# Optimization experiments

Measured on AMD Instinct MI355X. Metric: run time of the kernel, lower is better.

## Reference

```python
import jax, jax.numpy as jnp
import numpy as np

WEIGHT = 1.0  # config['weight']


def setup_inputs() -> dict:
    key = jax.random.key(0)
    ks = jax.random.split(key, 10)
    B, N, S, C, D, E, H, V = 8, 4096, 512, 16, 1024, 256, 1024, 100000
    return {
        "span_vecs": jax.random.normal(ks[0], (B, N, D), jnp.float32),
        "ent_table": jax.random.normal(ks[1], (V, E), jnp.float32) * 0.02,
        "W1": jax.random.normal(ks[2], (D + E, H), jnp.float32) * (1.0 / np.sqrt(D + E)),
        "b1": jnp.zeros((H,), jnp.float32),
        "W2": jax.random.normal(ks[3], (H,), jnp.float32) * (1.0 / np.sqrt(H)),
        "b2": jnp.zeros((), jnp.float32),
        "targets_all": jax.random.uniform(ks[4], (B, N, C), jnp.float32),
        "linker_indices": jax.random.randint(ks[5], (B, S), 0, N, jnp.int32),
        "candidates_all": jax.random.randint(ks[6], (B, N, C), 0, V, jnp.int32),
        "candidate_lengths_all": jax.random.randint(ks[7], (B, N), 0, C + 1, jnp.int32),
    }


def reference(span_vecs, ent_table, W1, b1, W2, b2, targets_all,
              linker_indices, candidates_all, candidate_lengths_all):
    D = span_vecs.shape[-1]
    C = candidates_all.shape[-1]
    idx = linker_indices  # [B, S]

    # batched_index_select gathers over the span axis
    candidates = jnp.take_along_axis(candidates_all, idx[:, :, None], axis=1)        # [B,S,C] int
    lengths = jnp.take_along_axis(candidate_lengths_all, idx, axis=1)                # [B,S] int
    targets = jnp.take_along_axis(targets_all, idx[:, :, None], axis=1)              # [B,S,C]
    linker_vecs = jnp.take_along_axis(span_vecs, idx[:, :, None], axis=1)            # [B,S,D]

    cand_vecs = ent_table[candidates]                                                # [B,S,C,E]

    # layers: Linear(D+E,H) -> ReLU -> (dropout=identity in eval) -> Linear(H,1)
    # fused: split W1 so the [B,S,C,D+E] expanded concat is never materialized
    W1s, W1e = W1[:D], W1[D:]
    h_span = jnp.einsum('bsd,dh->bsh', linker_vecs, W1s)                             # [B,S,H]
    h_cand = jnp.einsum('bsce,eh->bsch', cand_vecs, W1e)                             # [B,S,C,H]
    h = jax.nn.relu(h_span[:, :, None, :] + h_cand + b1)
    scores = jnp.einsum('bsch,h->bsc', h, W2) + b2                                   # [B,S,C]

    # create_candidate_mask
    mask = (jnp.arange(C)[None, None, :] < lengths[:, :, None]).astype(scores.dtype)

    # BCEWithLogitsLoss(reduction='none'), masked sum * weight
    bce = jnp.maximum(scores, 0.0) - scores * targets + jnp.log1p(jnp.exp(-jnp.abs(scores)))
    loss = (mask * bce).sum() * WEIGHT

    predictions = jnp.argmax(scores - (1.0 - mask) * 1e23, axis=-1)                  # [B,S]
    return loss, scores, predictions
```

## Files before the change

### kernel.cpp

```cpp
#include <hip/hip_runtime.h>
#include <math.h>


typedef short short8 __attribute__((ext_vector_type(8)));
typedef _Float16 half8v __attribute__((ext_vector_type(8)));
typedef float f32x16 __attribute__((ext_vector_type(16)));

static __device__ inline unsigned short f2bf(float x) {
  unsigned u = __float_as_uint(x);
  unsigned r = (u + 0x7FFFu + ((u >> 16) & 1u)) >> 16;
  return (unsigned short)r;
}
static __device__ inline float bf2f(unsigned short b) {
  return __uint_as_float(((unsigned)b) << 16);
}
static __device__ inline unsigned short f2h(float x) {
  _Float16 h = (_Float16)x;
  return *(unsigned short*)&h;
}

#define GLD_TO_LDS(gp, lp)                                          \
  __builtin_amdgcn_global_load_lds(                                 \
      (const __attribute__((address_space(1))) void*)(gp),          \
      (__attribute__((address_space(3))) void*)(lp), 16, 0, 0)

__global__ __launch_bounds__(256) void k_prep2(const int* __restrict__ linker,
                                               const int* __restrict__ cand_all,
                                               int* __restrict__ cand_ids,
                                               int* __restrict__ span_rows) {
  int g = blockIdx.x * 256 + threadIdx.x;
  int pair = g >> 4;
  int b = pair >> 9;
  int i = linker[pair];
  cand_ids[g] = cand_all[(((size_t)b << 12) + (size_t)i) * 16 + (g & 15)];
  if (g < 4096) span_rows[g] = ((g >> 9) << 12) + linker[g];
}

template <int LOG4>
__global__ __launch_bounds__(256) void k_gsplit(const float* __restrict__ src,
                                                const int* __restrict__ rows,
                                                unsigned short* __restrict__ hi,
                                                unsigned short* __restrict__ lo) {
  int f = blockIdx.x * 256 + threadIdx.x;
  int row = f >> LOG4;
  int c4 = f & ((1 << LOG4) - 1);
  const float4 v =
      *((const float4*)(src + ((size_t)rows[row] << (LOG4 + 2))) + c4);
  unsigned short h0 = f2bf(v.x), h1 = f2bf(v.y), h2 = f2bf(v.z), h3 = f2bf(v.w);
  unsigned short l0 = f2bf(v.x - bf2f(h0)), l1 = f2bf(v.y - bf2f(h1));
  unsigned short l2 = f2bf(v.z - bf2f(h2)), l3 = f2bf(v.w - bf2f(h3));
  *(ushort4*)(hi + ((size_t)f << 2)) = make_ushort4(h0, h1, h2, h3);
  *(ushort4*)(lo + ((size_t)f << 2)) = make_ushort4(l0, l1, l2, l3);
}

template <int LOG4>
__global__ __launch_bounds__(256) void k_gh(const float* __restrict__ src,
                                            const int* __restrict__ rows,
                                            unsigned short* __restrict__ dst) {
  int f = blockIdx.x * 256 + threadIdx.x;
  int row = f >> LOG4;
  int c4 = f & ((1 << LOG4) - 1);
  const float4 v =
      *((const float4*)(src + ((size_t)rows[row] << (LOG4 + 2))) + c4);
  *(ushort4*)(dst + ((size_t)f << 2)) =
      make_ushort4(f2h(v.x), f2h(v.y), f2h(v.z), f2h(v.w));
}

__global__ __launch_bounds__(256) void k_w1t(const float* __restrict__ W1,
                                             unsigned short* __restrict__ sThi,
                                             unsigned short* __restrict__ sTlo,
                                             unsigned short* __restrict__ eT16) {
  __shared__ float t[32][33];
  int n0 = blockIdx.x * 32, k0 = blockIdx.y * 32;
  int rr = threadIdx.x >> 5, cc = threadIdx.x & 31;
#pragma unroll
  for (int i = 0; i < 4; ++i)
    t[rr + 8 * i][cc] = W1[(size_t)(k0 + rr + 8 * i) * 1024 + n0 + cc];
  __syncthreads();
#pragma unroll
  for (int i = 0; i < 4; ++i) {
    int nl = rr + 8 * i;
    float v = t[cc][nl];
    int n = n0 + nl, k = k0 + cc;
    if (k0 < 1024) {
      unsigned short h = f2bf(v);
      unsigned short l = f2bf(v - bf2f(h));
      sThi[(size_t)n * 1024 + k] = h;
      sTlo[(size_t)n * 1024 + k] = l;
    } else {
      eT16[(size_t)n * 256 + (k - 1024)] = f2h(v);
    }
  }
}

template <int KSTEPS, int RLA, int RLB>
__global__ __launch_bounds__(256, 2) void k_g32(
    const unsigned short* __restrict__ Ahi, const unsigned short* __restrict__ Alo,
    const unsigned short* __restrict__ Bhi, const unsigned short* __restrict__ Blo,
    float* __restrict__ Out) {
  const int tid = threadIdx.x;
  const int l = tid & 63;
  const int w = tid >> 6;
  const int wm = w >> 1, wn = w & 1;
  const int id = blockIdx.x;
  const int m8 = id & 7;
  const int cb = (id >> 3) & 7;
  const int q = id >> 6;
  const int row0 = ((q << 3) + m8) << 7;
  const int col0 = cb << 7;

  __shared__ unsigned short lds[32768];

  f32x16 acc[2][2];
#pragma unroll
  for (int i = 0; i < 2; ++i)
#pragma unroll
    for (int j = 0; j < 2; ++j)
#pragma unroll
      for (int k = 0; k < 16; ++k) acc[i][j][k] = 0.f;

  const int ar0 = tid >> 2, ap0 = tid & 3;
  const int al0c = ap0 ^ ((ar0 >> 1) & 3);
  const int ar1 = (tid + 256) >> 2;
  const int al1c = ap0 ^ ((ar1 >> 1) & 3);
  const size_t aoff0 = (size_t)(row0 + ar0) * RLA + al0c * 8;
  const size_t aoff1 = (size_t)(row0 + ar1) * RLA + al1c * 8;
  const size_t boff0 = (size_t)(col0 + ar0) * RLB + al0c * 8;
  const size_t boff1 = (size_t)(col0 + ar1) * RLB + al1c * 8;
  const int w512 = w * 512;

  {
    unsigned short* b = lds;
    GLD_TO_LDS(Ahi + aoff0, b + w512);
    GLD_TO_LDS(Ahi + aoff1, b + 2048 + w512);
    GLD_TO_LDS(Alo + aoff0, b + 4096 + w512);
    GLD_TO_LDS(Alo + aoff1, b + 6144 + w512);
    GLD_TO_LDS(Bhi + boff0, b + 8192 + w512);
    GLD_TO_LDS(Bhi + boff1, b + 10240 + w512);
    GLD_TO_LDS(Blo + boff0, b + 12288 + w512);
    GLD_TO_LDS(Blo + boff1, b + 14336 + w512);
  }
  asm volatile("s_waitcnt vmcnt(0)" ::: "memory");
  __builtin_amdgcn_s_barrier();
  asm volatile("" ::: "memory");

  for (int ks = 0; ks < KSTEPS; ++ks) {
    if (ks + 1 < KSTEPS) {
      const int k0 = (ks + 1) * 32;
      unsigned short* b = lds + (((ks + 1) & 1) << 14);
      GLD_TO_LDS(Ahi + aoff0 + k0, b + w512);
      GLD_TO_LDS(Ahi + aoff1 + k0, b + 2048 + w512);
      GLD_TO_LDS(Alo + aoff0 + k0, b + 4096 + w512);
      GLD_TO_LDS(Alo + aoff1 + k0, b + 6144 + w512);
      GLD_TO_LDS(Bhi + boff0 + k0, b + 8192 + w512);
      GLD_TO_LDS(Bhi + boff1 + k0, b + 10240 + w512);
      GLD_TO_LDS(Blo + boff0 + k0, b + 12288 + w512);
      GLD_TO_LDS(Blo + boff1 + k0, b + 14336 + w512);
    }

    const unsigned short* cbuf = lds + ((ks & 1) << 14);
#pragma unroll
    for (int kc = 0; kc < 2; ++kc) {
      const int kg = kc * 2 + (l >> 5);
      short8 ah[2], alv[2], bh[2], bl[2];
#pragma unroll
      for (int it = 0; it < 2; ++it) {
        int r = wm * 64 + it * 32 + (l & 31);
        int off = r * 32 + ((kg ^ ((r >> 1) & 3)) << 3);
        ah[it] = *(const short8*)(cbuf + off);
        alv[it] = *(const short8*)(cbuf + 4096 + off);
      }
#pragma unroll
      for (int jt = 0; jt < 2; ++jt) {
        int r = wn * 64 + jt * 32 + (l & 31);
        int off = r * 32 + ((kg ^ ((r >> 1) & 3)) << 3);
        bh[jt] = *(const short8*)(cbuf + 8192 + off);
        bl[jt] = *(const short8*)(cbuf + 12288 + off);
      }
#pragma unroll
      for (int it = 0; it < 2; ++it)
#pragma unroll
        for (int jt = 0; jt < 2; ++jt) {
          acc[it][jt] = __builtin_amdgcn_mfma_f32_32x32x16_bf16(
              ah[it], bh[jt], acc[it][jt], 0, 0, 0);
          acc[it][jt] = __builtin_amdgcn_mfma_f32_32x32x16_bf16(
              ah[it], bl[jt], acc[it][jt], 0, 0, 0);
          acc[it][jt] = __builtin_amdgcn_mfma_f32_32x32x16_bf16(
              alv[it], bh[jt], acc[it][jt], 0, 0, 0);
        }
    }

    if (ks + 1 < KSTEPS) {
      asm volatile("s_waitcnt vmcnt(0)" ::: "memory");
      __builtin_amdgcn_s_barrier();
      asm volatile("" ::: "memory");
    }
  }

#pragma unroll
  for (int it = 0; it < 2; ++it) {
    int mb = row0 + wm * 64 + it * 32 + 4 * (l >> 5);
#pragma unroll
    for (int jt = 0; jt < 2; ++jt) {
      int n = col0 + wn * 64 + jt * 32 + (l & 31);
#pragma unroll
      for (int rg = 0; rg < 16; ++rg) {
        int m = mb + (rg & 3) + 8 * (rg >> 2);
        Out[(size_t)m * 1024 + n] = acc[it][jt][rg];
      }
    }
  }
}

__global__ __launch_bounds__(256, 4) void k_gf16(
    const unsigned short* __restrict__ A,
    const unsigned short* __restrict__ Bt,
    const float* __restrict__ HsIn, const float* __restrict__ b1,
    const float* __restrict__ W2, float* __restrict__ Out) {
  const int tid = threadIdx.x;
  const int l = tid & 63;
  const int w = tid >> 6;
  const int wm = w >> 1, wn = w & 1;
  const int id = blockIdx.x;
  const int m8 = id & 7;
  const int cb = (id >> 3) & 7;
  const int q = id >> 6;
  const int row0 = ((q << 3) + m8) << 7;
  const int col0 = cb << 7;

  __shared__ unsigned short lds[16384];

  f32x16 acc[2][2];
#pragma unroll
  for (int i = 0; i < 2; ++i)
#pragma unroll
    for (int j = 0; j < 2; ++j)
#pragma unroll
      for (int k = 0; k < 16; ++k) acc[i][j][k] = 0.f;

  const int ar0 = tid >> 2, ap0 = tid & 3;
  const int al0c = ap0 ^ ((ar0 >> 1) & 3);
  const int ar1 = (tid + 256) >> 2;
  const int al1c = ap0 ^ ((ar1 >> 1) & 3);
  const size_t aoff0 = (size_t)(row0 + ar0) * 256 + al0c * 8;
  const size_t aoff1 = (size_t)(row0 + ar1) * 256 + al1c * 8;
  const size_t boff0 = (size_t)(col0 + ar0) * 256 + al0c * 8;
  const size_t boff1 = (size_t)(col0 + ar1) * 256 + al1c * 8;
  const int w512 = w * 512;

  GLD_TO_LDS(A + aoff0, lds + w512);
  GLD_TO_LDS(A + aoff1, lds + 2048 + w512);
  GLD_TO_LDS(Bt + boff0, lds + 4096 + w512);
  GLD_TO_LDS(Bt + boff1, lds + 6144 + w512);
  asm volatile("s_waitcnt vmcnt(0)" ::: "memory");
  __builtin_amdgcn_s_barrier();
  asm volatile("" ::: "memory");

#pragma unroll 2
  for (int ks = 0; ks < 8; ++ks) {
    if (ks + 1 < 8) {
      const int k0 = (ks + 1) * 32;
      unsigned short* b = lds + (((ks + 1) & 1) << 13);
      GLD_TO_LDS(A + aoff0 + k0, b + w512);
      GLD_TO_LDS(A + aoff1 + k0, b + 2048 + w512);
      GLD_TO_LDS(Bt + boff0 + k0, b + 4096 + w512);
      GLD_TO_LDS(Bt + boff1 + k0, b + 6144 + w512);
    }

    const unsigned short* cbuf = lds + ((ks & 1) << 13);
#pragma unroll
    for (int kc = 0; kc < 2; ++kc) {
      const int kg = kc * 2 + (l >> 5);
      half8v av[2], bv[2];
#pragma unroll
      for (int it = 0; it < 2; ++it) {
        int r = wm * 64 + it * 32 + (l & 31);
        int off = r * 32 + ((kg ^ ((r >> 1) & 3)) << 3);
        av[it] = *(const half8v*)(cbuf + off);
      }
#pragma unroll
      for (int jt = 0; jt < 2; ++jt) {
        int r = wn * 64 + jt * 32 + (l & 31);
        int off = r * 32 + ((kg ^ ((r >> 1) & 3)) << 3);
        bv[jt] = *(const half8v*)(cbuf + 4096 + off);
      }
#pragma unroll
      for (int it = 0; it < 2; ++it)
#pragma unroll
        for (int jt = 0; jt < 2; ++jt)
          acc[it][jt] = __builtin_amdgcn_mfma_f32_32x32x16_f16(
              av[it], bv[jt], acc[it][jt], 0, 0, 0);
    }

    if (ks + 1 < 8) {
      asm volatile("s_waitcnt vmcnt(0)" ::: "memory");
      __builtin_amdgcn_s_barrier();
      asm volatile("" ::: "memory");
    }
  }

  float sv[2][16];
#pragma unroll
  for (int it = 0; it < 2; ++it) {
#pragma unroll
    for (int rg = 0; rg < 16; ++rg) sv[it][rg] = 0.f;
    const int p0 = (row0 + wm * 64 + it * 32) >> 4;
#pragma unroll
    for (int jt = 0; jt < 2; ++jt) {
      int n = col0 + wn * 64 + jt * 32 + (l & 31);
      float b1v = b1[n], w2v = W2[n];
      float add0 = HsIn[(size_t)p0 * 1024 + n] + b1v;
      float add1 = HsIn[(size_t)(p0 + 1) * 1024 + n] + b1v;
#pragma unroll
      for (int rg = 0; rg < 16; ++rg) {
        float h = fmaxf(acc[it][jt][rg] + (rg < 8 ? add0 : add1), 0.f);
        sv[it][rg] = fmaf(h, w2v, sv[it][rg]);
      }
    }
  }
  __syncthreads();
  float* scf = (float*)lds;
  const int cc0 = l & 31, lh4 = 4 * (l >> 5);
#pragma unroll
  for (int it = 0; it < 2; ++it)
#pragma unroll
    for (int rg = 0; rg < 16; ++rg) {
      int row = (rg & 3) + 8 * (rg >> 2) + lh4;
      scf[((w * 2 + it) * 32 + row) * 32 + ((cc0 + row) & 31)] = sv[it][rg];
    }
  __syncthreads();
  int gr = tid >> 1, h = tid & 1;
  int r = gr & 31, itv = (gr >> 5) & 1, wmv = gr >> 6;
  const float* sa = scf + ((wmv * 4 + itv) * 32 + r) * 32;
  const float* sb = scf + ((wmv * 4 + 2 + itv) * 32 + r) * 32;
  float sum = 0.f;
#pragma unroll
  for (int j = 0; j < 16; ++j) {
    int cidx = (h * 16 + j + r) & 31;
    sum += sa[cidx] + sb[cidx];
  }
  sum += __shfl_xor(sum, 1, 64);
  if (h == 0) Out[(size_t)cb * 65536 + row0 + gr] = sum;
}

__global__ __launch_bounds__(64) void k_final8(const float* __restrict__ score8,
                                               const float* __restrict__ b2p,
                                               const float* __restrict__ targets_all,
                                               const int* __restrict__ linker,
                                               const int* __restrict__ len_all,
                                               float* __restrict__ out) {
  int p = blockIdx.x * 64 + threadIdx.x;
  float b2 = b2p[0];
  int b = p >> 9;
  int i = linker[p];
  int len = len_all[(b << 12) + i];
  const float* tg = targets_all + ((((size_t)b << 12) + (size_t)i) << 4);

  float loss = 0.f;
  float best = -INFINITY;
  int bc = 0;
#pragma unroll
  for (int c = 0; c < 16; ++c) {
    float sc = b2;
#pragma unroll
    for (int c8 = 0; c8 < 8; ++c8) sc += score8[c8 * 65536 + p * 16 + c];
    out[1 + p * 16 + c] = sc;
    float val;
    if (c < len) {
      float t = tg[c];
      loss += fmaxf(sc, 0.f) - sc * t + log1pf(expf(-fabsf(sc)));
      val = sc;
    } else {
      val = sc - 1e23f;
    }
    if (val > best) { best = val; bc = c; }
  }
  out[1 + 65536 + p] = (float)bc;

  for (int off = 32; off > 0; off >>= 1) loss += __shfl_down(loss, off, 64);
  if (threadIdx.x == 0) atomicAdd(out, loss);
}

#define BM 128
#define BN 128
#define BK 16
#define PAD 4

__global__ __launch_bounds__(256) void k_prep(const int* __restrict__ linker,
                                              const int* __restrict__ cand_all,
                                              int* __restrict__ cand_ids) {
  int g = blockIdx.x * 256 + threadIdx.x;
  int pair = g >> 4;
  int c = g & 15;
  int b = pair >> 9;
  int i = linker[pair];
  cand_ids[g] = cand_all[(((size_t)b << 12) + (size_t)i) * 16 + c];
}

__global__ __launch_bounds__(256) void k_hs(const float* __restrict__ span,
                                            const float* __restrict__ W1,
                                            const int* __restrict__ linker,
                                            float* __restrict__ Hs) {
  const int tid = threadIdx.x;
  const int tx = tid & 15, ty = tid >> 4;
  const int row0 = blockIdx.y * BM;
  const int col0 = blockIdx.x * BN;
  __shared__ float As[BK][BM + PAD];
  __shared__ float Bs[BK][BN + PAD];
  __shared__ int rows_g[BM];
  if (tid < BM) {
    int m = row0 + tid;
    int b = m >> 9;
    rows_g[tid] = (b << 12) + linker[m];
  }
  __syncthreads();
  float acc[8][8] = {};
  for (int k0 = 0; k0 < 1024; k0 += BK) {
#pragma unroll
    for (int ll = 0; ll < 2; ++ll) {
      int f = tid + ll * 256;
      int r = f >> 2;
      int kk = (f & 3) << 2;
      const float4 v = *(const float4*)(span + (size_t)rows_g[r] * 1024 + k0 + kk);
      As[kk + 0][r] = v.x; As[kk + 1][r] = v.y;
      As[kk + 2][r] = v.z; As[kk + 3][r] = v.w;
    }
#pragma unroll
    for (int ll = 0; ll < 2; ++ll) {
      int f = tid + ll * 256;
      int kk = f >> 5;
      int nn = (f & 31) << 2;
      *(float4*)&Bs[kk][nn] = *(const float4*)(W1 + (size_t)(k0 + kk) * 1024 + col0 + nn);
    }
    __syncthreads();
#pragma unroll
    for (int k = 0; k < BK; ++k) {
      float a[8], b[8];
      *(float4*)&a[0] = *(const float4*)&As[k][ty * 8];
      *(float4*)&a[4] = *(const float4*)&As[k][ty * 8 + 4];
      *(float4*)&b[0] = *(const float4*)&Bs[k][tx * 8];
      *(float4*)&b[4] = *(const float4*)&Bs[k][tx * 8 + 4];
#pragma unroll
      for (int i = 0; i < 8; ++i)
#pragma unroll
        for (int j = 0; j < 8; ++j) acc[i][j] = fmaf(a[i], b[j], acc[i][j]);
    }
    __syncthreads();
  }
#pragma unroll
  for (int i = 0; i < 8; ++i) {
    int m = row0 + ty * 8 + i;
    float* dst = Hs + (size_t)m * 1024 + col0 + tx * 8;
    *(float4*)dst = *(float4*)&acc[i][0];
    *(float4*)(dst + 4) = *(float4*)&acc[i][4];
  }
}

__global__ __launch_bounds__(256) void k_hc(const float* __restrict__ ent,
                                            const float* __restrict__ W1,
                                            const int* __restrict__ cand_ids,
                                            const float* __restrict__ Hs,
                                            const float* __restrict__ b1,
                                            const float* __restrict__ W2,
                                            float* __restrict__ score_ws) {
  const int tid = threadIdx.x;
  const int tx = tid & 15, ty = tid >> 4;
  const int row0 = blockIdx.y * BM;
  const int col0 = blockIdx.x * BN;
  __shared__ float As[BK][BM + PAD];
  __shared__ float Bs[BK][BN + PAD];
  __shared__ int rows_g[BM];
  __shared__ float red[BM][17];
  if (tid < BM) rows_g[tid] = cand_ids[row0 + tid];
  __syncthreads();
  float acc[8][8] = {};
  for (int k0 = 0; k0 < 256; k0 += BK) {
#pragma unroll
    for (int ll = 0; ll < 2; ++ll) {
      int f = tid + ll * 256;
      int r = f >> 2;
      int kk = (f & 3) << 2;
      const float4 v = *(const float4*)(ent + (size_t)rows_g[r] * 256 + k0 + kk);
      As[kk + 0][r] = v.x; As[kk + 1][r] = v.y;
      As[kk + 2][r] = v.z; As[kk + 3][r] = v.w;
    }
#pragma unroll
    for (int ll = 0; ll < 2; ++ll) {
      int f = tid + ll * 256;
      int kk = f >> 5;
      int nn = (f & 31) << 2;
      *(float4*)&Bs[kk][nn] =
          *(const float4*)(W1 + (size_t)(1024 + k0 + kk) * 1024 + col0 + nn);
    }
    __syncthreads();
#pragma unroll
    for (int k = 0; k < BK; ++k) {
      float a[8], b[8];
      *(float4*)&a[0] = *(const float4*)&As[k][ty * 8];
      *(float4*)&a[4] = *(const float4*)&As[k][ty * 8 + 4];
      *(float4*)&b[0] = *(const float4*)&Bs[k][tx * 8];
      *(float4*)&b[4] = *(const float4*)&Bs[k][tx * 8 + 4];
#pragma unroll
      for (int i = 0; i < 8; ++i)
#pragma unroll
        for (int j = 0; j < 8; ++j) acc[i][j] = fmaf(a[i], b[j], acc[i][j]);
    }
    __syncthreads();
  }
  const int pair = (row0 + ty * 8) >> 4;
  float hsv[8], b1v[8], w2v[8];
  {
    const float* hp = Hs + (size_t)pair * 1024 + col0 + tx * 8;
    *(float4*)&hsv[0] = *(const float4*)hp;
    *(float4*)&hsv[4] = *(const float4*)(hp + 4);
    const float* bp = b1 + col0 + tx * 8;
    *(float4*)&b1v[0] = *(const float4*)bp;
    *(float4*)&b1v[4] = *(const float4*)(bp + 4);
    const float* wp = W2 + col0 + tx * 8;
    *(float4*)&w2v[0] = *(const float4*)wp;
    *(float4*)&w2v[4] = *(const float4*)(wp + 4);
  }
#pragma unroll
  for (int i = 0; i < 8; ++i) {
    float s = 0.f;
#pragma unroll
    for (int j = 0; j < 8; ++j) {
      float h = acc[i][j] + hsv[j] + b1v[j];
      h = fmaxf(h, 0.f);
      s = fmaf(h, w2v[j], s);
    }
    red[ty * 8 + i][tx] = s;
  }
  __syncthreads();
  if (tid < BM) {
    float s = 0.f;
#pragma unroll
    for (int x = 0; x < 16; ++x) s += red[tid][x];
    atomicAdd(&score_ws[row0 + tid], s);
  }
}

__global__ __launch_bounds__(256) void k_final(const float* __restrict__ score_ws,
                                               const float* __restrict__ b2p,
                                               const float* __restrict__ targets_all,
                                               const int* __restrict__ linker,
                                               const int* __restrict__ len_all,
                                               float* __restrict__ out) {
  int p = blockIdx.x * 256 + threadIdx.x;
  float b2 = b2p[0];
  int b = p >> 9;
  int i = linker[p];
  int len = len_all[(b << 12) + i];
  const float* tg = targets_all + ((((size_t)b << 12) + (size_t)i) << 4);

  float loss = 0.f;
  float best = -INFINITY;
  int bc = 0;
#pragma unroll
  for (int c = 0; c < 16; ++c) {
    float sc = score_ws[p * 16 + c] + b2;
    out[1 + p * 16 + c] = sc;
    float val;
    if (c < len) {
      float t = tg[c];
      loss += fmaxf(sc, 0.f) - sc * t + log1pf(expf(-fabsf(sc)));
      val = sc;
    } else {
      val = sc - 1e23f;
    }
    if (val > best) { best = val; bc = c; }
  }
  out[1 + 65536 + p] = (float)bc;

  for (int off = 32; off > 0; off >>= 1) loss += __shfl_down(loss, off, 64);
  if ((threadIdx.x & 63) == 0) atomicAdd(out, loss);
}

extern "C" void kernel_launch(void* const* d_in, const int* in_sizes, int n_in,
                              void* d_out, int out_size, void* d_ws,
                              size_t ws_size, hipStream_t stream) {
  const float* span    = (const float*)d_in[0];
  const float* ent     = (const float*)d_in[1];
  const float* W1      = (const float*)d_in[2];
  const float* b1      = (const float*)d_in[3];
  const float* W2      = (const float*)d_in[4];
  const float* b2      = (const float*)d_in[5];
  const float* targets = (const float*)d_in[6];
  const int* linker    = (const int*)d_in[7];
  const int* cand_all  = (const int*)d_in[8];
  const int* len_all   = (const int*)d_in[9];
  float* out = (float*)d_out;

  char* ws = (char*)d_ws;
  float* Hs       = (float*)(ws + 0);
  float* score_ws = (float*)(ws + 16777216);
  int* cand_ids   = (int*)(ws + 17039360);
  int* span_rows  = (int*)(ws + 17301504);
  unsigned short* A1h  = (unsigned short*)(ws + 17317888);
  unsigned short* A1l  = (unsigned short*)(ws + 25706496);
  unsigned short* A2   = (unsigned short*)(ws + 34095104);
  unsigned short* sTh  = (unsigned short*)(ws + 101203968);
  unsigned short* sTl  = (unsigned short*)(ws + 103301120);
  unsigned short* eT16 = (unsigned short*)(ws + 105398272);
  const size_t NEED_MFMA = 106446848;
  float* score8 = (float*)A1h;

  hipMemsetAsync(d_out, 0, sizeof(float), stream);

  if (ws_size >= NEED_MFMA) {
    k_prep2<<<dim3(256), dim3(256), 0, stream>>>(linker, cand_all, cand_ids,
                                                 span_rows);
    k_gh<6><<<dim3(16384), dim3(256), 0, stream>>>(ent, cand_ids, A2);
    k_gsplit<8><<<dim3(4096), dim3(256), 0, stream>>>(span, span_rows, A1h, A1l);
    k_w1t<<<dim3(32, 40), dim3(256), 0, stream>>>(W1, sTh, sTl, eT16);
    k_g32<32, 1024, 1024><<<dim3(256), dim3(256), 0, stream>>>(
        A1h, A1l, sTh, sTl, Hs);
    k_gf16<<<dim3(4096), dim3(256), 0, stream>>>(A2, eT16, Hs, b1, W2, score8);
    k_final8<<<dim3(64), dim3(64), 0, stream>>>(score8, b2, targets, linker,
                                                len_all, out);
  } else {
    hipMemsetAsync(score_ws, 0, 65536 * sizeof(float), stream);
    k_prep<<<dim3(256), dim3(256), 0, stream>>>(linker, cand_all, cand_ids);
    dim3 g1(8, 32);
    k_hs<<<g1, dim3(256), 0, stream>>>(span, W1, linker, Hs);
    dim3 g2(8, 512);
    k_hc<<<g2, dim3(256), 0, stream>>>(ent, W1, cand_ids, Hs, b1, W2, score_ws);
    k_final<<<dim3(16), dim3(256), 0, stream>>>(score_ws, b2, targets, linker,
                                                len_all, out);
  }
}
```

Measured before the change: 344.7 us.

## Merge prep kernels into one launch and split-K the span GEMM across two halves

Four preprocessing kernels (index gather, entity gather to fp16, span gather with bf16 hi/lo split, W1 transpose) are folded into one block-range-dispatched kernel, so the separate index-prep pass and three launches go away. The span GEMM is split along K into two halves with 512 blocks instead of 256, which fills more CUs. The two partial Hs outputs are summed in the candidate GEMM's epilogue, which adds an extra Hs buffer read. k_final8 now reads its score partials as float4 vectors.

```diff
diff --git a/kernel.cpp b/kernel.cpp
--- a/kernel.cpp
+++ b/kernel.cpp
@@ -24,71 +24,57 @@
       (const __attribute__((address_space(1))) void*)(gp),          \
       (__attribute__((address_space(3))) void*)(lp), 16, 0, 0)
 
-__global__ __launch_bounds__(256) void k_prep2(const int* __restrict__ linker,
-                                               const int* __restrict__ cand_all,
-                                               int* __restrict__ cand_ids,
-                                               int* __restrict__ span_rows) {
-  int g = blockIdx.x * 256 + threadIdx.x;
-  int pair = g >> 4;
-  int b = pair >> 9;
-  int i = linker[pair];
-  cand_ids[g] = cand_all[(((size_t)b << 12) + (size_t)i) * 16 + (g & 15)];
-  if (g < 4096) span_rows[g] = ((g >> 9) << 12) + linker[g];
-}
-
-template <int LOG4>
-__global__ __launch_bounds__(256) void k_gsplit(const float* __restrict__ src,
-                                                const int* __restrict__ rows,
-                                                unsigned short* __restrict__ hi,
-                                                unsigned short* __restrict__ lo) {
-  int f = blockIdx.x * 256 + threadIdx.x;
-  int row = f >> LOG4;
-  int c4 = f & ((1 << LOG4) - 1);
-  const float4 v =
-      *((const float4*)(src + ((size_t)rows[row] << (LOG4 + 2))) + c4);
-  unsigned short h0 = f2bf(v.x), h1 = f2bf(v.y), h2 = f2bf(v.z), h3 = f2bf(v.w);
-  unsigned short l0 = f2bf(v.x - bf2f(h0)), l1 = f2bf(v.y - bf2f(h1));
-  unsigned short l2 = f2bf(v.z - bf2f(h2)), l3 = f2bf(v.w - bf2f(h3));
-  *(ushort4*)(hi + ((size_t)f << 2)) = make_ushort4(h0, h1, h2, h3);
-  *(ushort4*)(lo + ((size_t)f << 2)) = make_ushort4(l0, l1, l2, l3);
-}
-
-template <int LOG4>
-__global__ __launch_bounds__(256) void k_gh(const float* __restrict__ src,
-                                            const int* __restrict__ rows,
-                                            unsigned short* __restrict__ dst) {
-  int f = blockIdx.x * 256 + threadIdx.x;
-  int row = f >> LOG4;
-  int c4 = f & ((1 << LOG4) - 1);
-  const float4 v =
-      *((const float4*)(src + ((size_t)rows[row] << (LOG4 + 2))) + c4);
-  *(ushort4*)(dst + ((size_t)f << 2)) =
-      make_ushort4(f2h(v.x), f2h(v.y), f2h(v.z), f2h(v.w));
-}
-
-__global__ __launch_bounds__(256) void k_w1t(const float* __restrict__ W1,
-                                             unsigned short* __restrict__ sThi,
-                                             unsigned short* __restrict__ sTlo,
-                                             unsigned short* __restrict__ eT16) {
+__global__ __launch_bounds__(256) void k_prep_all(
+    const float* __restrict__ span, const float* __restrict__ ent,
+    const float* __restrict__ W1, const int* __restrict__ linker,
+    const int* __restrict__ cand_all, unsigned short* __restrict__ A1h,
+    unsigned short* __restrict__ A1l, unsigned short* __restrict__ A2,
+    unsigned short* __restrict__ sThi, unsigned short* __restrict__ sTlo,
+    unsigned short* __restrict__ eT16) {
   __shared__ float t[32][33];
-  int n0 = blockIdx.x * 32, k0 = blockIdx.y * 32;
-  int rr = threadIdx.x >> 5, cc = threadIdx.x & 31;
-#pragma unroll
-  for (int i = 0; i < 4; ++i)
-    t[rr + 8 * i][cc] = W1[(size_t)(k0 + rr + 8 * i) * 1024 + n0 + cc];
-  __syncthreads();
-#pragma unroll
-  for (int i = 0; i < 4; ++i) {
-    int nl = rr + 8 * i;
-    float v = t[cc][nl];
-    int n = n0 + nl, k = k0 + cc;
-    if (k0 < 1024) {
-      unsigned short h = f2bf(v);
-      unsigned short l = f2bf(v - bf2f(h));
-      sThi[(size_t)n * 1024 + k] = h;
-      sTlo[(size_t)n * 1024 + k] = l;
-    } else {
-      eT16[(size_t)n * 256 + (k - 1024)] = f2h(v);
+  const int bx = blockIdx.x;
+  if (bx < 16384) {
+    int f = bx * 256 + threadIdx.x;
+    int row = f >> 6;
+    int pair = row >> 4;
+    int b = pair >> 9;
+    int i = linker[pair];
+    int cid = cand_all[(((size_t)b << 12) + (size_t)i) * 16 + (row & 15)];
+    const float4 v = *((const float4*)(ent + ((size_t)cid << 8)) + (f & 63));
+    *(ushort4*)(A2 + ((size_t)f << 2)) =
+        make_ushort4(f2h(v.x), f2h(v.y), f2h(v.z), f2h(v.w));
+  } else if (bx < 20480) {
+    int f = (bx - 16384) * 256 + threadIdx.x;
+    int row = f >> 8;
+    int b = row >> 9;
+    int srow = (b << 12) + linker[row];
+    const float4 v = *((const float4*)(span + ((size_t)srow << 10)) + (f & 255));
+    unsigned short h0 = f2bf(v.x), h1 = f2bf(v.y), h2 = f2bf(v.z), h3 = f2bf(v.w);
+    unsigned short l0 = f2bf(v.x - bf2f(h0)), l1 = f2bf(v.y - bf2f(h1));
+    unsigned short l2 = f2bf(v.z - bf2f(h2)), l3 = f2bf(v.w - bf2f(h3));
+    *(ushort4*)(A1h + ((size_t)f << 2)) = make_ushort4(h0, h1, h2, h3);
+    *(ushort4*)(A1l + ((size_t)f << 2)) = make_ushort4(l0, l1, l2, l3);
+  } else {
+    int b2x = bx - 20480;
+    int n0 = (b2x & 31) * 32, k0 = (b2x >> 5) * 32;
+    int rr = threadIdx.x >> 5, cc = threadIdx.x & 31;
+#pragma unroll
+    for (int i = 0; i < 4; ++i)
+      t[rr + 8 * i][cc] = W1[(size_t)(k0 + rr + 8 * i) * 1024 + n0 + cc];
+    __syncthreads();
+#pragma unroll
+    for (int i = 0; i < 4; ++i) {
+      int nl = rr + 8 * i;
+      float v = t[cc][nl];
+      int n = n0 + nl, k = k0 + cc;
+      if (k0 < 1024) {
+        unsigned short h = f2bf(v);
+        unsigned short l = f2bf(v - bf2f(h));
+        sThi[(size_t)n * 1024 + k] = h;
+        sTlo[(size_t)n * 1024 + k] = l;
+      } else {
+        eT16[(size_t)n * 256 + (k - 1024)] = f2h(v);
+      }
     }
   }
 }
@@ -103,11 +89,15 @@
   const int w = tid >> 6;
   const int wm = w >> 1, wn = w & 1;
   const int id = blockIdx.x;
-  const int m8 = id & 7;
-  const int cb = (id >> 3) & 7;
-  const int q = id >> 6;
+  const int z = id >> 8;
+  const int sid = id & 255;
+  const int m8 = sid & 7;
+  const int cb = (sid >> 3) & 7;
+  const int q = sid >> 6;
   const int row0 = ((q << 3) + m8) << 7;
   const int col0 = cb << 7;
+  const int koff = z * (KSTEPS * 32);
+  Out += (size_t)z * 4194304;
 
   __shared__ unsigned short lds[32768];
 
@@ -123,10 +113,10 @@
   const int al0c = ap0 ^ ((ar0 >> 1) & 3);
   const int ar1 = (tid + 256) >> 2;
   const int al1c = ap0 ^ ((ar1 >> 1) & 3);
-  const size_t aoff0 = (size_t)(row0 + ar0) * RLA + al0c * 8;
-  const size_t aoff1 = (size_t)(row0 + ar1) * RLA + al1c * 8;
-  const size_t boff0 = (size_t)(col0 + ar0) * RLB + al0c * 8;
-  const size_t boff1 = (size_t)(col0 + ar1) * RLB + al1c * 8;
+  const size_t aoff0 = (size_t)(row0 + ar0) * RLA + al0c * 8 + koff;
+  const size_t aoff1 = (size_t)(row0 + ar1) * RLA + al1c * 8 + koff;
+  const size_t boff0 = (size_t)(col0 + ar0) * RLB + al0c * 8 + koff;
+  const size_t boff1 = (size_t)(col0 + ar1) * RLB + al1c * 8 + koff;
   const int w512 = w * 512;
 
   {
@@ -309,8 +299,10 @@
     for (int jt = 0; jt < 2; ++jt) {
       int n = col0 + wn * 64 + jt * 32 + (l & 31);
       float b1v = b1[n], w2v = W2[n];
-      float add0 = HsIn[(size_t)p0 * 1024 + n] + b1v;
-      float add1 = HsIn[(size_t)(p0 + 1) * 1024 + n] + b1v;
+      float add0 = HsIn[(size_t)p0 * 1024 + n] +
+                   HsIn[4194304 + (size_t)p0 * 1024 + n] + b1v;
+      float add1 = HsIn[(size_t)(p0 + 1) * 1024 + n] +
+                   HsIn[4194304 + (size_t)(p0 + 1) * 1024 + n] + b1v;
 #pragma unroll
       for (int rg = 0; rg < 16; ++rg) {
         float h = fmaxf(acc[it][jt][rg] + (rg < 8 ? add0 : add1), 0.f);
@@ -356,22 +348,34 @@
   int len = len_all[(b << 12) + i];
   const float* tg = targets_all + ((((size_t)b << 12) + (size_t)i) << 4);
 
+  float sc[16];
+#pragma unroll
+  for (int c = 0; c < 16; ++c) sc[c] = b2;
+#pragma unroll
+  for (int c8 = 0; c8 < 8; ++c8) {
+    const float4* q4 = (const float4*)(score8 + (size_t)c8 * 65536 + p * 16);
+#pragma unroll
+    for (int j = 0; j < 4; ++j) {
+      float4 v = q4[j];
+      sc[j * 4 + 0] += v.x; sc[j * 4 + 1] += v.y;
+      sc[j * 4 + 2] += v.z; sc[j * 4 + 3] += v.w;
+    }
+  }
+
   float loss = 0.f;
   float best = -INFINITY;
   int bc = 0;
 #pragma unroll
   for (int c = 0; c < 16; ++c) {
-    float sc = b2;
-#pragma unroll
-    for (int c8 = 0; c8 < 8; ++c8) sc += score8[c8 * 65536 + p * 16 + c];
-    out[1 + p * 16 + c] = sc;
+    float s = sc[c];
+    out[1 + p * 16 + c] = s;
     float val;
     if (c < len) {
       float t = tg[c];
-      loss += fmaxf(sc, 0.f) - sc * t + log1pf(expf(-fabsf(sc)));
-      val = sc;
+      loss += fmaxf(s, 0.f) - s * t + log1pf(expf(-fabsf(s)));
+      val = s;
     } else {
-      val = sc - 1e23f;
+      val = s - 1e23f;
     }
     if (val > best) { best = val; bc = c; }
   }
@@ -593,27 +597,23 @@
 
   char* ws = (char*)d_ws;
   float* Hs       = (float*)(ws + 0);
-  float* score_ws = (float*)(ws + 16777216);
-  int* cand_ids   = (int*)(ws + 17039360);
-  int* span_rows  = (int*)(ws + 17301504);
-  unsigned short* A1h  = (unsigned short*)(ws + 17317888);
-  unsigned short* A1l  = (unsigned short*)(ws + 25706496);
-  unsigned short* A2   = (unsigned short*)(ws + 34095104);
-  unsigned short* sTh  = (unsigned short*)(ws + 101203968);
-  unsigned short* sTl  = (unsigned short*)(ws + 103301120);
-  unsigned short* eT16 = (unsigned short*)(ws + 105398272);
-  const size_t NEED_MFMA = 106446848;
+  float* score_ws = (float*)(ws + 33554432);
+  int* cand_ids   = (int*)(ws + 33816576 + 8388608);
+  unsigned short* A1h  = (unsigned short*)(ws + 33816576);
+  unsigned short* A1l  = (unsigned short*)(ws + 42205184);
+  unsigned short* A2   = (unsigned short*)(ws + 50593792);
+  unsigned short* sTh  = (unsigned short*)(ws + 84148224);
+  unsigned short* sTl  = (unsigned short*)(ws + 86245376);
+  unsigned short* eT16 = (unsigned short*)(ws + 88342528);
+  const size_t NEED_MFMA = 88866816;
   float* score8 = (float*)A1h;
 
   hipMemsetAsync(d_out, 0, sizeof(float), stream);
 
   if (ws_size >= NEED_MFMA) {
-    k_prep2<<<dim3(256), dim3(256), 0, stream>>>(linker, cand_all, cand_ids,
-                                                 span_rows);
-    k_gh<6><<<dim3(16384), dim3(256), 0, stream>>>(ent, cand_ids, A2);
-    k_gsplit<8><<<dim3(4096), dim3(256), 0, stream>>>(span, span_rows, A1h, A1l);
-    k_w1t<<<dim3(32, 40), dim3(256), 0, stream>>>(W1, sTh, sTl, eT16);
-    k_g32<32, 1024, 1024><<<dim3(256), dim3(256), 0, stream>>>(
+    k_prep_all<<<dim3(21760), dim3(256), 0, stream>>>(
+        span, ent, W1, linker, cand_all, A1h, A1l, A2, sTh, sTl, eT16);
+    k_g32<16, 1024, 1024><<<dim3(512), dim3(256), 0, stream>>>(
         A1h, A1l, sTh, sTl, Hs);
     k_gf16<<<dim3(4096), dim3(256), 0, stream>>>(A2, eT16, Hs, b1, W2, score8);
     k_final8<<<dim3(64), dim3(64), 0, stream>>>(score8, b2, targets, linker,
```

New measurement: 337.7 us. 2.0% less time.
